# Kernel optimization log

Hardware: AMD Instinct MI355X
Metric: run time of the kernel (lower is better)

Reference implementation:

```python
import jax, jax.numpy as jnp
import numpy as np

B, N, F, C, K = 4, 8192, 128, 64, 16


def setup_inputs() -> dict:
    key = jax.random.key(0)
    ks = jax.random.split(key, 24)
    s = 0.05
    rn = lambda k, shape: (jax.random.normal(k, shape, jnp.float32) * s)
    return {
        "features": jax.random.normal(ks[0], (B, N, F), jnp.float32),
        "positions": jax.random.normal(ks[1], (B, N, 3), jnp.float32),
        "batch": jnp.repeat(jnp.arange(B, dtype=jnp.int32), N),
        "num_neighbors": K,
        # linear encoder (F -> C)
        "W_enc": rn(ks[2], (F, C)), "b_enc": jnp.zeros((C,), jnp.float32),
        # point-transformer q/k/v projections (C -> C)
        "Wq": rn(ks[3], (C, C)), "bq": jnp.zeros((C,), jnp.float32),
        "Wk": rn(ks[4], (C, C)), "bk": jnp.zeros((C,), jnp.float32),
        "Wv": rn(ks[5], (C, C)), "bv": jnp.zeros((C,), jnp.float32),
        # positional encoding MLP: 3 -> C -> C (ReLU)
        "Wp1": rn(ks[6], (3, C)), "bp1": jnp.zeros((C,), jnp.float32),
        "Wp2": rn(ks[7], (C, C)), "bp2": jnp.zeros((C,), jnp.float32),
        # attention MLP gamma: C -> C -> C (ReLU)
        "Wa1": rn(ks[8], (C, C)), "ba1": jnp.zeros((C,), jnp.float32),
        "Wa2": rn(ks[9], (C, C)), "ba2": jnp.zeros((C,), jnp.float32),
        # linear decoder (C -> F)
        "W_dec": rn(ks[10], (C, F)), "b_dec": jnp.zeros((F,), jnp.float32),
    }


def reference(features, positions, batch, num_neighbors,
              W_enc, b_enc, Wq, bq, Wk, bk, Wv, bv,
              Wp1, bp1, Wp2, bp2, Wa1, ba1, Wa2, ba2, W_dec, b_dec):
    # linear encode: [B,N,F] -> [B,N,C]
    x = features @ W_enc + b_enc
    q = x @ Wq + bq
    k = x @ Wk + bk
    v = x @ Wv + bv

    def per_cloud(pos, qi, ki, vi):
        # kNN via pairwise squared distances (self included, dist 0)
        sq = jnp.sum(pos * pos, axis=-1)                      # [N]
        d2 = sq[:, None] + sq[None, :] - 2.0 * (pos @ pos.T)  # [N,N]
        idx = jax.lax.top_k(-d2, num_neighbors)[1]            # [N,K]
        kj = ki[idx]                                          # [N,K,C] gather
        vj = vi[idx]                                          # [N,K,C]
        rel = pos[:, None, :] - pos[idx]                      # [N,K,3]
        # positional encoding delta = MLP(p_i - p_j)
        delta = jax.nn.relu(rel @ Wp1 + bp1) @ Wp2 + bp2      # [N,K,C]
        # vector attention: gamma(q_i - k_j + delta), softmax over K neighbors
        a = qi[:, None, :] - kj + delta
        a = jax.nn.relu(a @ Wa1 + ba1) @ Wa2 + ba2
        w = jax.nn.softmax(a, axis=1)                         # [N,K,C]
        return jnp.sum(w * (vj + delta), axis=1)              # [N,C]

    y = jax.vmap(per_cloud)(positions, q, k, v)               # [B,N,C]
    out = y @ W_dec + b_dec + features                        # decode + residual
    return (out, positions, batch)
```

## Files before the change

kernel.cpp:

```cpp
#include <hip/hip_runtime.h>
#include <hip/hip_bf16.h>

#define NPTS 32768
#define NPC  8192
#define KNN  16
#define CH   64
#define FDIM 128
#define EMPTYKEY 0x7F7FFFFFu

typedef __bf16 bf16;
typedef __bf16 bf16x8 __attribute__((ext_vector_type(8)));
typedef float  f32x4  __attribute__((ext_vector_type(4)));

__global__ __launch_bounds__(256) void k_encode(
    const float* __restrict__ feat,
    const float* __restrict__ Wenc, const float* __restrict__ benc,
    const float* __restrict__ Wq, const float* __restrict__ bq,
    const float* __restrict__ Wk, const float* __restrict__ bk,
    const float* __restrict__ Wv, const float* __restrict__ bv,
    float* __restrict__ qo, float* __restrict__ ko, float* __restrict__ vo)
{
    __shared__ float xs[4][CH];
    int t = threadIdx.x;
    int c = t & 63, pl = t >> 6;
    size_t pt = (size_t)blockIdx.x * 4 + pl;
    const float* fr = feat + pt * FDIM;
    float acc = benc[c];
#pragma unroll 8
    for (int f4 = 0; f4 < 32; ++f4) {
        float4 fv = *reinterpret_cast<const float4*>(fr + f4 * 4);
        acc += fv.x * Wenc[(f4*4+0)*CH + c];
        acc += fv.y * Wenc[(f4*4+1)*CH + c];
        acc += fv.z * Wenc[(f4*4+2)*CH + c];
        acc += fv.w * Wenc[(f4*4+3)*CH + c];
    }
    xs[pl][c] = acc;
    __syncthreads();
    float aq = bq[c], ak = bk[c], av = bv[c];
#pragma unroll 4
    for (int m = 0; m < CH; ++m) {
        float xm = xs[pl][m];
        aq += xm * Wq[m*CH + c];
        ak += xm * Wk[m*CH + c];
        av += xm * Wv[m*CH + c];
    }
    qo[pt*CH + c] = aq; ko[pt*CH + c] = ak; vo[pt*CH + c] = av;
}

__global__ __launch_bounds__(256, 4) void k_knn(
    const float* __restrict__ pos, unsigned* __restrict__ wsK)
{
    __shared__ float4 sp[1024];
    __shared__ unsigned sbuf[256 * 17];

    int t = threadIdx.x;
    int blk = blockIdx.x;
    int slice = blk & 7;
    int qg = (blk >> 3) & 31;
    int cloud = blk >> 8;
    const float* pc = pos + (size_t)cloud * NPC * 3;
    int jbase = slice << 10;

    {
        const float4* src = reinterpret_cast<const float4*>(pc + (size_t)jbase * 3);
        float4 a = src[t*3+0], b1 = src[t*3+1], c1 = src[t*3+2];
        sp[t*4+0] = make_float4(a.x,  a.y,  a.z,  0.f);
        sp[t*4+1] = make_float4(a.w,  b1.x, b1.y, 0.f);
        sp[t*4+2] = make_float4(b1.z, b1.w, c1.x, 0.f);
        sp[t*4+3] = make_float4(c1.y, c1.z, c1.w, 0.f);
    }
    __syncthreads();

    int qi = (qg << 8) + t;
    float myx = pc[qi*3+0], myy = pc[qi*3+1], myz = pc[qi*3+2];

    unsigned arr[16];
#pragma unroll
    for (int r = 0; r < 16; ++r) arr[r] = EMPTYKEY;
    float thrf = __uint_as_float(EMPTYKEY & 0xFFFFE000u);
    int cnt = 0;
    int base = t * 17;

    for (int g = 0; g < 1024; g += 4) {
        float d2v[4];
#pragma unroll
        for (int u = 0; u < 4; ++u) {
            float4 p = sp[g + u];
            float dx = myx - p.x, dy = myy - p.y, dz = myz - p.z;
            d2v[u] = dx*dx + dy*dy + dz*dz;
        }
        float m4 = fminf(fminf(d2v[0], d2v[1]), fminf(d2v[2], d2v[3]));
        if (__any(m4 <= thrf)) {
#pragma unroll
            for (int u = 0; u < 4; ++u) {
                if (d2v[u] <= thrf) {
                    sbuf[base + cnt] = (__float_as_uint(d2v[u]) & 0xFFFFE000u)
                                       | (unsigned)(jbase + g + u);
                    ++cnt;
                }
            }
            if (__any(cnt >= 13)) {
#pragma unroll
                for (int b = 0; b < 16; ++b) {
                    unsigned key = (b < cnt) ? sbuf[base + b] : EMPTYKEY;
#pragma unroll
                    for (int r = 0; r < 16; ++r) {
                        unsigned lo = min(key, arr[r]);
                        unsigned hi = max(key, arr[r]);
                        arr[r] = lo; key = hi;
                    }
                }
                cnt = 0;
                thrf = __uint_as_float(arr[15] & 0xFFFFE000u);
            }
        }
    }
#pragma unroll
    for (int b = 0; b < 16; ++b) {
        unsigned key = (b < cnt) ? sbuf[base + b] : EMPTYKEY;
#pragma unroll
        for (int r = 0; r < 16; ++r) {
            unsigned lo = min(key, arr[r]);
            unsigned hi = max(key, arr[r]);
            arr[r] = lo; key = hi;
        }
    }
    unsigned* o = wsK + (((size_t)(cloud * NPC + qi)) * 8 + slice) * 16;
#pragma unroll
    for (int r = 0; r < 16; ++r) o[r] = arr[r];
}

__global__ __launch_bounds__(64) void k_merge(
    const unsigned* __restrict__ wsK, int* __restrict__ idxout)
{
    __shared__ unsigned kk[64][137];
    int t = threadIdx.x;
    size_t q = (size_t)blockIdx.x * 64 + t;
    const uint4* src = reinterpret_cast<const uint4*>(wsK + q * 128);
#pragma unroll
    for (int i = 0; i < 32; ++i) {
        uint4 v = src[i];
        int w = i * 4;
        int s = (w >> 4) * 17 + (w & 15);
        kk[t][s] = v.x; kk[t][s+1] = v.y; kk[t][s+2] = v.z; kk[t][s+3] = v.w;
    }
#pragma unroll
    for (int l = 0; l < 8; ++l) kk[t][l*17 + 16] = 0xFFFFFFFFu;

    unsigned h0=0,h1=0,h2=0,h3=0,h4=0,h5=0,h6=0,h7=0;
    int* o = idxout + q * KNN;
    for (int r = 0; r < KNN; ++r) {
        unsigned best = 0xFFFFFFFFu; int bl = 0; unsigned k;
        k = kk[t][0*17 + h0]; if (k < best) { best = k; bl = 0; }
        k = kk[t][1*17 + h1]; if (k < best) { best = k; bl = 1; }
        k = kk[t][2*17 + h2]; if (k < best) { best = k; bl = 2; }
        k = kk[t][3*17 + h3]; if (k < best) { best = k; bl = 3; }
        k = kk[t][4*17 + h4]; if (k < best) { best = k; bl = 4; }
        k = kk[t][5*17 + h5]; if (k < best) { best = k; bl = 5; }
        k = kk[t][6*17 + h6]; if (k < best) { best = k; bl = 6; }
        k = kk[t][7*17 + h7]; if (k < best) { best = k; bl = 7; }
        o[r] = (int)(best & 0x1FFFu);
        h0 += (bl == 0); h1 += (bl == 1); h2 += (bl == 2); h3 += (bl == 3);
        h4 += (bl == 4); h5 += (bl == 5); h6 += (bl == 6); h7 += (bl == 7);
    }
}

__global__ __launch_bounds__(64) void k_pack(
    const float* __restrict__ Wp2, const float* __restrict__ Wa1,
    const float* __restrict__ Wa2, bf16* __restrict__ wpk)
{
    int lane = threadIdx.x;
    int mlane = lane & 15, kgrp = lane >> 4;
    const float* Ws[3] = {Wp2, Wa1, Wa2};
    bf16x8* o = reinterpret_cast<bf16x8*>(wpk);
    for (int gmm = 0; gmm < 3; ++gmm) {
#pragma unroll
        for (int nt = 0; nt < 4; ++nt) {
#pragma unroll
            for (int kt = 0; kt < 2; ++kt) {
                bf16x8 v;
#pragma unroll
                for (int j = 0; j < 8; ++j)
                    v[j] = (bf16)Ws[gmm][(kt*32 + kgrp*8 + j)*CH + nt*16 + mlane];
                o[(gmm*8 + nt*2 + kt)*64 + lane] = v;
            }
        }
    }
}

__device__ __forceinline__ void wave_gemm(
    const bf16* At, f32x4 acc[4][4], const bf16x8* __restrict__ wpk,
    int w, int lane)
{
    int kgrp = lane >> 4;
    bf16x8 wf[4][2];
#pragma unroll
    for (int nt = 0; nt < 4; ++nt)
#pragma unroll
        for (int kt = 0; kt < 2; ++kt)
            wf[nt][kt] = wpk[(nt*2 + kt)*64 + lane];
#pragma unroll
    for (int mt = 0; mt < 4; ++mt) {
        int row = w*64 + mt*16 + (lane & 15);
        const bf16* rb = At + row*CH;
        int sw = row & 7;
        bf16x8 a0 = *reinterpret_cast<const bf16x8*>(rb + ((kgrp     ^ sw) * 8));
        bf16x8 a1 = *reinterpret_cast<const bf16x8*>(rb + (((4+kgrp) ^ sw) * 8));
#pragma unroll
        for (int nt = 0; nt < 4; ++nt) {
            acc[mt][nt] = __builtin_amdgcn_mfma_f32_16x16x32_bf16(a0, wf[nt][0], acc[mt][nt], 0, 0, 0);
            acc[mt][nt] = __builtin_amdgcn_mfma_f32_16x16x32_bf16(a1, wf[nt][1], acc[mt][nt], 0, 0, 0);
        }
    }
}

__global__ __launch_bounds__(128) void k_attn(
    const float* __restrict__ pos, const int* __restrict__ nidx,
    const float* __restrict__ qg, const float* __restrict__ kg, const float* __restrict__ vg,
    const float* __restrict__ Wp1, const float* __restrict__ bp1,
    const float* __restrict__ bp2, const float* __restrict__ ba1,
    const float* __restrict__ ba2, const bf16* __restrict__ wpkg,
    float* __restrict__ yout)
{
    __shared__ bf16 At[128 * CH];
    __shared__ bf16 Vt[128 * CH];

    int t = threadIdx.x;
    int w = t >> 6, lane = t & 63;
    int mlane = lane & 15, kgrp = lane >> 4;
    size_t p0 = (size_t)blockIdx.x * 8;
    size_t cbase = (p0 >> 13) << 13;
    const bf16x8* wpk = reinterpret_cast<const bf16x8*>(wpkg);

    {
        int p = t >> 4, j = t & 15;
        size_t gp = p0 + p;
        int nbr = nidx[gp*KNN + j];
        size_t gn = cbase + (size_t)nbr;
        float rx = pos[gp*3+0] - pos[gn*3+0];
        float ry = pos[gp*3+1] - pos[gn*3+1];
        float rz = pos[gp*3+2] - pos[gn*3+2];
        float h[CH];
#pragma unroll
        for (int c4 = 0; c4 < 16; ++c4) {
            float4 w0 = *reinterpret_cast<const float4*>(Wp1 + 0*CH + c4*4);
            float4 w1 = *reinterpret_cast<const float4*>(Wp1 + 1*CH + c4*4);
            float4 w2 = *reinterpret_cast<const float4*>(Wp1 + 2*CH + c4*4);
            float4 bb = *reinterpret_cast<const float4*>(bp1 + c4*4);
            h[c4*4+0] = fmaxf(rx*w0.x + ry*w1.x + rz*w2.x + bb.x, 0.f);
            h[c4*4+1] = fmaxf(rx*w0.y + ry*w1.y + rz*w2.y + bb.y, 0.f);
            h[c4*4+2] = fmaxf(rx*w0.z + ry*w1.z + rz*w2.z + bb.z, 0.f);
            h[c4*4+3] = fmaxf(rx*w0.w + ry*w1.w + rz*w2.w + bb.w, 0.f);
        }
#pragma unroll
        for (int ch = 0; ch < 8; ++ch) {
            bf16x8 v;
#pragma unroll
            for (int e = 0; e < 8; ++e) v[e] = (bf16)h[ch*8 + e];
            *reinterpret_cast<bf16x8*>(&At[t*CH + (ch ^ (t & 7)) * 8]) = v;
        }
    }

    f32x4 acc[4][4];

#pragma unroll
    for (int nt = 0; nt < 4; ++nt) {
        float b = bp2[nt*16 + mlane];
#pragma unroll
        for (int mt = 0; mt < 4; ++mt) { acc[mt][nt][0]=b; acc[mt][nt][1]=b; acc[mt][nt][2]=b; acc[mt][nt][3]=b; }
    }
    wave_gemm(At, acc, wpk, w, lane);

#pragma unroll
    for (int mt = 0; mt < 4; ++mt) {
        size_t gp = p0 + (size_t)(w*4 + mt);
        int nb[4];
#pragma unroll
        for (int reg = 0; reg < 4; ++reg)
            nb[reg] = nidx[gp*KNN + kgrp*4 + reg];
#pragma unroll
        for (int nt = 0; nt < 4; ++nt) {
            int c = nt*16 + mlane;
            float qv = qg[gp*CH + c];
#pragma unroll
            for (int reg = 0; reg < 4; ++reg) {
                float dlt = acc[mt][nt][reg];
                size_t gr = cbase + (size_t)nb[reg];
                float kv = kg[gr*CH + c];
                float vv = vg[gr*CH + c];
                int row = w*64 + mt*16 + kgrp*4 + reg;
                int off = row*CH + (((c >> 3) ^ (row & 7)) * 8) + (c & 7);
                At[off] = (bf16)(qv - kv + dlt);
                Vt[off] = (bf16)(vv + dlt);
            }
        }
    }

#pragma unroll
    for (int nt = 0; nt < 4; ++nt) {
        float b = ba1[nt*16 + mlane];
#pragma unroll
        for (int mt = 0; mt < 4; ++mt) { acc[mt][nt][0]=b; acc[mt][nt][1]=b; acc[mt][nt][2]=b; acc[mt][nt][3]=b; }
    }
    wave_gemm(At, acc, wpk + 512, w, lane);
#pragma unroll
    for (int mt = 0; mt < 4; ++mt) {
#pragma unroll
        for (int nt = 0; nt < 4; ++nt) {
            int c = nt*16 + mlane;
#pragma unroll
            for (int reg = 0; reg < 4; ++reg) {
                int row = w*64 + mt*16 + kgrp*4 + reg;
                int off = row*CH + (((c >> 3) ^ (row & 7)) * 8) + (c & 7);
                At[off] = (bf16)fmaxf(acc[mt][nt][reg], 0.f);
            }
        }
    }

#pragma unroll
    for (int nt = 0; nt < 4; ++nt) {
        float b = ba2[nt*16 + mlane];
#pragma unroll
        for (int mt = 0; mt < 4; ++mt) { acc[mt][nt][0]=b; acc[mt][nt][1]=b; acc[mt][nt][2]=b; acc[mt][nt][3]=b; }
    }
    wave_gemm(At, acc, wpk + 1024, w, lane);

#pragma unroll
    for (int mt = 0; mt < 4; ++mt) {
        size_t gp = p0 + (size_t)(w*4 + mt);
#pragma unroll
        for (int nt = 0; nt < 4; ++nt) {
            int c = nt*16 + mlane;
            float m = fmaxf(fmaxf(acc[mt][nt][0], acc[mt][nt][1]),
                            fmaxf(acc[mt][nt][2], acc[mt][nt][3]));
            m = fmaxf(m, __shfl_xor(m, 16));
            m = fmaxf(m, __shfl_xor(m, 32));
            float e[4], s = 0.f;
#pragma unroll
            for (int reg = 0; reg < 4; ++reg) { e[reg] = __expf(acc[mt][nt][reg] - m); s += e[reg]; }
            s += __shfl_xor(s, 16);
            s += __shfl_xor(s, 32);
            float num = 0.f;
#pragma unroll
            for (int reg = 0; reg < 4; ++reg) {
                int row = w*64 + mt*16 + kgrp*4 + reg;
                int off = row*CH + (((c >> 3) ^ (row & 7)) * 8) + (c & 7);
                num += e[reg] * (float)Vt[off];
            }
            num += __shfl_xor(num, 16);
            num += __shfl_xor(num, 32);
            if (kgrp == 0) yout[gp*CH + c] = num / s;
        }
    }
}

__global__ __launch_bounds__(256) void k_decode(
    const float* __restrict__ y, const float* __restrict__ Wd, const float* __restrict__ bd,
    const float* __restrict__ feat, float* __restrict__ out)
{
    int t = threadIdx.x;
    int f = t & 127, pl = t >> 7;
    size_t pt = (size_t)blockIdx.x * 2 + pl;
    const float* yr = y + pt*CH;
    float acc = bd[f] + feat[pt*FDIM + f];
#pragma unroll
    for (int c4 = 0; c4 < 16; ++c4) {
        float4 yv = *reinterpret_cast<const float4*>(yr + c4*4);
        acc += yv.x * Wd[(c4*4+0)*FDIM + f];
        acc += yv.y * Wd[(c4*4+1)*FDIM + f];
        acc += yv.z * Wd[(c4*4+2)*FDIM + f];
        acc += yv.w * Wd[(c4*4+3)*FDIM + f];
    }
    out[pt*FDIM + f] = acc;
}

__global__ void k_tail(const float* __restrict__ pos, const int* __restrict__ batch,
                       float* __restrict__ outtail)
{
    int i = blockIdx.x * 256 + threadIdx.x;
    if (i < NPTS*3) outtail[i] = pos[i];
    if (i < NPTS)   outtail[NPTS*3 + i] = (float)batch[i];
}

extern "C" void kernel_launch(void* const* d_in, const int* in_sizes, int n_in,
                              void* d_out, int out_size, void* d_ws, size_t ws_size,
                              hipStream_t stream)
{
    const float* feat  = (const float*)d_in[0];
    const float* pos   = (const float*)d_in[1];
    const int*   batch = (const int*)d_in[2];
    const float* Wenc  = (const float*)d_in[4];
    const float* benc  = (const float*)d_in[5];
    const float* Wq = (const float*)d_in[6];   const float* bq = (const float*)d_in[7];
    const float* Wk = (const float*)d_in[8];   const float* bk = (const float*)d_in[9];
    const float* Wv = (const float*)d_in[10];  const float* bv = (const float*)d_in[11];
    const float* Wp1= (const float*)d_in[12];  const float* bp1= (const float*)d_in[13];
    const float* Wp2= (const float*)d_in[14];  const float* bp2= (const float*)d_in[15];
    const float* Wa1= (const float*)d_in[16];  const float* ba1= (const float*)d_in[17];
    const float* Wa2= (const float*)d_in[18];  const float* ba2= (const float*)d_in[19];
    const float* Wd = (const float*)d_in[20];  const float* bd = (const float*)d_in[21];
    float* out = (float*)d_out;

    int*      idx = (int*)d_ws;
    unsigned* wsK = (unsigned*)((char*)d_ws + (size_t)NPTS*KNN*sizeof(int));
    float* qb = (float*)wsK;
    float* kb = qb + (size_t)NPTS*CH;
    float* vb = kb + (size_t)NPTS*CH;
    float* yb = vb + (size_t)NPTS*CH;
    bf16*  wpk = (bf16*)(yb + (size_t)NPTS*CH);

    k_knn<<<1024, 256, 0, stream>>>(pos, wsK);
    k_merge<<<NPTS/64, 64, 0, stream>>>(wsK, idx);
    k_pack<<<1, 64, 0, stream>>>(Wp2, Wa1, Wa2, wpk);

    k_encode<<<NPTS/4, 256, 0, stream>>>(feat, Wenc, benc, Wq, bq, Wk, bk, Wv, bv, qb, kb, vb);

    k_attn<<<NPTS/8, 128, 0, stream>>>(pos, idx, qb, kb, vb,
                                       Wp1, bp1, bp2, ba1, ba2, wpk, yb);

    k_decode<<<NPTS/2, 256, 0, stream>>>(yb, Wd, bd, feat, out);

    k_tail<<<(NPTS*3 + 255)/256, 256, 0, stream>>>(pos, batch, out + (size_t)NPTS*FDIM);
}
```

Baseline: 466.4 us.

## Transpose kNN candidate layout, fuse small kernels, keep V+delta in registers

Stores per-slice kNN candidates in a slice-major layout so writes in k_knn and reads in k_merge coalesce across query points. Folds weight packing into k_merge and the position/batch tail copy into k_decode to drop two launches. Replaces the Vt shared buffer in k_attn with packed bf16 registers, halving LDS and adding an occupancy hint of three blocks per CU. Register pressure rises, which may cause spills under the new launch bound.

```diff
diff --git a/kernel.cpp b/kernel.cpp
--- a/kernel.cpp
+++ b/kernel.cpp
@@ -9,6 +9,7 @@
 #define EMPTYKEY 0x7F7FFFFFu
 
 typedef __bf16 bf16;
+typedef __bf16 bf16x2 __attribute__((ext_vector_type(2)));
 typedef __bf16 bf16x8 __attribute__((ext_vector_type(8)));
 typedef float  f32x4  __attribute__((ext_vector_type(4)));
 
@@ -125,27 +126,26 @@
             arr[r] = lo; key = hi;
         }
     }
-    unsigned* o = wsK + (((size_t)(cloud * NPC + qi)) * 8 + slice) * 16;
-#pragma unroll
-    for (int r = 0; r < 16; ++r) o[r] = arr[r];
+    size_t gq = (size_t)cloud * NPC + qi;
+#pragma unroll
+    for (int r = 0; r < 16; ++r) wsK[(size_t)(slice*16 + r)*NPTS + gq] = arr[r];
 }
 
 __global__ __launch_bounds__(64) void k_merge(
-    const unsigned* __restrict__ wsK, int* __restrict__ idxout)
+    const unsigned* __restrict__ wsK, int* __restrict__ idxout,
+    const float* __restrict__ Wp2, const float* __restrict__ Wa1,
+    const float* __restrict__ Wa2, bf16* __restrict__ wpk)
 {
     __shared__ unsigned kk[64][137];
     int t = threadIdx.x;
     size_t q = (size_t)blockIdx.x * 64 + t;
-    const uint4* src = reinterpret_cast<const uint4*>(wsK + q * 128);
-#pragma unroll
-    for (int i = 0; i < 32; ++i) {
-        uint4 v = src[i];
-        int w = i * 4;
-        int s = (w >> 4) * 17 + (w & 15);
-        kk[t][s] = v.x; kk[t][s+1] = v.y; kk[t][s+2] = v.z; kk[t][s+3] = v.w;
-    }
-#pragma unroll
-    for (int l = 0; l < 8; ++l) kk[t][l*17 + 16] = 0xFFFFFFFFu;
+#pragma unroll
+    for (int l = 0; l < 8; ++l) {
+#pragma unroll
+        for (int r = 0; r < 16; ++r)
+            kk[t][l*17 + r] = wsK[(size_t)(l*16 + r)*NPTS + q];
+        kk[t][l*17 + 16] = 0xFFFFFFFFu;
+    }
 
     unsigned h0=0,h1=0,h2=0,h3=0,h4=0,h5=0,h6=0,h7=0;
     int* o = idxout + q * KNN;
@@ -163,26 +163,23 @@
         h0 += (bl == 0); h1 += (bl == 1); h2 += (bl == 2); h3 += (bl == 3);
         h4 += (bl == 4); h5 += (bl == 5); h6 += (bl == 6); h7 += (bl == 7);
     }
-}
-
-__global__ __launch_bounds__(64) void k_pack(
-    const float* __restrict__ Wp2, const float* __restrict__ Wa1,
-    const float* __restrict__ Wa2, bf16* __restrict__ wpk)
-{
-    int lane = threadIdx.x;
-    int mlane = lane & 15, kgrp = lane >> 4;
-    const float* Ws[3] = {Wp2, Wa1, Wa2};
-    bf16x8* o = reinterpret_cast<bf16x8*>(wpk);
-    for (int gmm = 0; gmm < 3; ++gmm) {
-#pragma unroll
-        for (int nt = 0; nt < 4; ++nt) {
-#pragma unroll
-            for (int kt = 0; kt < 2; ++kt) {
-                bf16x8 v;
-#pragma unroll
-                for (int j = 0; j < 8; ++j)
-                    v[j] = (bf16)Ws[gmm][(kt*32 + kgrp*8 + j)*CH + nt*16 + mlane];
-                o[(gmm*8 + nt*2 + kt)*64 + lane] = v;
+
+    if (blockIdx.x == 0) {
+        int lane = t;
+        int mlane = lane & 15, kgrp = lane >> 4;
+        const float* Ws[3] = {Wp2, Wa1, Wa2};
+        bf16x8* ow = reinterpret_cast<bf16x8*>(wpk);
+        for (int gmm = 0; gmm < 3; ++gmm) {
+#pragma unroll
+            for (int nt = 0; nt < 4; ++nt) {
+#pragma unroll
+                for (int kt = 0; kt < 2; ++kt) {
+                    bf16x8 v;
+#pragma unroll
+                    for (int j = 0; j < 8; ++j)
+                        v[j] = (bf16)Ws[gmm][(kt*32 + kgrp*8 + j)*CH + nt*16 + mlane];
+                    ow[(gmm*8 + nt*2 + kt)*64 + lane] = v;
+                }
             }
         }
     }
@@ -214,7 +211,7 @@
     }
 }
 
-__global__ __launch_bounds__(128) void k_attn(
+__global__ __launch_bounds__(128, 3) void k_attn(
     const float* __restrict__ pos, const int* __restrict__ nidx,
     const float* __restrict__ qg, const float* __restrict__ kg, const float* __restrict__ vg,
     const float* __restrict__ Wp1, const float* __restrict__ bp1,
@@ -223,7 +220,6 @@
     float* __restrict__ yout)
 {
     __shared__ bf16 At[128 * CH];
-    __shared__ bf16 Vt[128 * CH];
 
     int t = threadIdx.x;
     int w = t >> 6, lane = t & 63;
@@ -271,6 +267,7 @@
     }
     wave_gemm(At, acc, wpk, w, lane);
 
+    bf16x2 vdp[4][4][2];
 #pragma unroll
     for (int mt = 0; mt < 4; ++mt) {
         size_t gp = p0 + (size_t)(w*4 + mt);
@@ -282,6 +279,7 @@
         for (int nt = 0; nt < 4; ++nt) {
             int c = nt*16 + mlane;
             float qv = qg[gp*CH + c];
+            float vdf[4];
 #pragma unroll
             for (int reg = 0; reg < 4; ++reg) {
                 float dlt = acc[mt][nt][reg];
@@ -291,8 +289,12 @@
                 int row = w*64 + mt*16 + kgrp*4 + reg;
                 int off = row*CH + (((c >> 3) ^ (row & 7)) * 8) + (c & 7);
                 At[off] = (bf16)(qv - kv + dlt);
-                Vt[off] = (bf16)(vv + dlt);
+                vdf[reg] = vv + dlt;
             }
+            bf16x2 lo2; lo2[0] = (bf16)vdf[0]; lo2[1] = (bf16)vdf[1];
+            bf16x2 hi2; hi2[0] = (bf16)vdf[2]; hi2[1] = (bf16)vdf[3];
+            vdp[mt][nt][0] = lo2;
+            vdp[mt][nt][1] = hi2;
         }
     }
 
@@ -341,12 +343,10 @@
             s += __shfl_xor(s, 16);
             s += __shfl_xor(s, 32);
             float num = 0.f;
-#pragma unroll
-            for (int reg = 0; reg < 4; ++reg) {
-                int row = w*64 + mt*16 + kgrp*4 + reg;
-                int off = row*CH + (((c >> 3) ^ (row & 7)) * 8) + (c & 7);
-                num += e[reg] * (float)Vt[off];
-            }
+            num += e[0] * (float)vdp[mt][nt][0][0];
+            num += e[1] * (float)vdp[mt][nt][0][1];
+            num += e[2] * (float)vdp[mt][nt][1][0];
+            num += e[3] * (float)vdp[mt][nt][1][1];
             num += __shfl_xor(num, 16);
             num += __shfl_xor(num, 32);
             if (kgrp == 0) yout[gp*CH + c] = num / s;
@@ -356,7 +356,8 @@
 
 __global__ __launch_bounds__(256) void k_decode(
     const float* __restrict__ y, const float* __restrict__ Wd, const float* __restrict__ bd,
-    const float* __restrict__ feat, float* __restrict__ out)
+    const float* __restrict__ feat, const float* __restrict__ pos,
+    const int* __restrict__ batch, float* __restrict__ out)
 {
     int t = threadIdx.x;
     int f = t & 127, pl = t >> 7;
@@ -372,14 +373,10 @@
         acc += yv.w * Wd[(c4*4+3)*FDIM + f];
     }
     out[pt*FDIM + f] = acc;
-}
-
-__global__ void k_tail(const float* __restrict__ pos, const int* __restrict__ batch,
-                       float* __restrict__ outtail)
-{
-    int i = blockIdx.x * 256 + threadIdx.x;
-    if (i < NPTS*3) outtail[i] = pos[i];
-    if (i < NPTS)   outtail[NPTS*3 + i] = (float)batch[i];
+
+    int i = blockIdx.x * 256 + t;
+    if (i < NPTS*3) out[(size_t)NPTS*FDIM + i] = pos[i];
+    if (i < NPTS)   out[(size_t)NPTS*FDIM + NPTS*3 + i] = (float)batch[i];
 }
 
 extern "C" void kernel_launch(void* const* d_in, const int* in_sizes, int n_in,
@@ -410,15 +407,12 @@
     bf16*  wpk = (bf16*)(yb + (size_t)NPTS*CH);
 
     k_knn<<<1024, 256, 0, stream>>>(pos, wsK);
-    k_merge<<<NPTS/64, 64, 0, stream>>>(wsK, idx);
-    k_pack<<<1, 64, 0, stream>>>(Wp2, Wa1, Wa2, wpk);
+    k_merge<<<NPTS/64, 64, 0, stream>>>(wsK, idx, Wp2, Wa1, Wa2, wpk);
 
     k_encode<<<NPTS/4, 256, 0, stream>>>(feat, Wenc, benc, Wq, bq, Wk, bk, Wv, bv, qb, kb, vb);
 
     k_attn<<<NPTS/8, 128, 0, stream>>>(pos, idx, qb, kb, vb,
                                        Wp1, bp1, bp2, ba1, ba2, wpk, yb);
 
-    k_decode<<<NPTS/2, 256, 0, stream>>>(yb, Wd, bd, feat, out);
-
-    k_tail<<<(NPTS*3 + 255)/256, 256, 0, stream>>>(pos, batch, out + (size_t)NPTS*FDIM);
-}
+    k_decode<<<NPTS/2, 256, 0, stream>>>(yb, Wd, bd, feat, pos, batch, out);
+}
```

After: 468.0 us. Within noise of the previous version (+0.4%).
